# Performance work log

Hardware: AMD Instinct MI355X
Metric: run time of the kernel (lower is better)

Reference implementation:

```python
import jax, jax.numpy as jnp
import numpy as np

SCALING = 2.0  # alpha / r = 128 / 64


def setup_inputs() -> dict:
    key = jax.random.key(0)
    k1, k2, k3, k4 = jax.random.split(key, 4)
    in_f, out_f, r, tokens = 4096, 16384, 64, 64
    return {
        "x": jax.random.normal(k1, (tokens, in_f), dtype=jnp.float32),
        "weight": jax.random.normal(k2, (out_f, in_f), dtype=jnp.float32) * (1.0 / np.sqrt(in_f)),
        "lora_A": jax.random.normal(k3, (r, in_f), dtype=jnp.float32) * (1.0 / np.sqrt(in_f)),
        "lora_B": jax.random.normal(k4, (out_f, r), dtype=jnp.float32) * (1.0 / np.sqrt(r)),
    }


def reference(x, weight, lora_A, lora_B):
    # base GEMM: [T, in] @ [in, out] -> [T, out]
    base = x @ weight.T
    # low-rank adapter: ((x @ A^T) @ B^T) scaled
    lora = (x @ lora_A.T) @ lora_B.T
    return base + SCALING * lora
```

## Files before the change

kernel.cpp:

```cpp
#include <hip/hip_runtime.h>
#include <hip/hip_bf16.h>

typedef __attribute__((ext_vector_type(8))) short bf16x8;
typedef __attribute__((ext_vector_type(4))) float f32x4;

__device__ __forceinline__ short f2b(float f) {
    __hip_bfloat16 h = __float2bfloat16(f);
    return __builtin_bit_cast(short, h);
}

#define NPH 32
#define KC  128

__global__ void prep_kernel(const float* __restrict__ x,
                            const float* __restrict__ A,
                            ushort* __restrict__ xb,
                            ushort* __restrict__ yb) {
    const int tid = threadIdx.x, bid = blockIdx.x;

    const int gid = bid * 256 + tid;
    if (gid < 65536) {
        float4 v = ((const float4*)x)[gid];
        ushort4 s;
        s.x = (ushort)f2b(v.x); s.y = (ushort)f2b(v.y);
        s.z = (ushort)f2b(v.z); s.w = (ushort)f2b(v.w);
        ((ushort4*)xb)[gid] = s;
    }

    const int wave = tid >> 6, lane = tid & 63;
    const int idx = bid * 4 + wave;
    const int t = idx >> 6, r = idx & 63;
    const float4* xr = (const float4*)(x + (size_t)t * 4096);
    const float4* ar = (const float4*)(A + (size_t)r * 4096);
    float s = 0.f;
    #pragma unroll
    for (int i = 0; i < 16; ++i) {
        float4 a = xr[i * 64 + lane];
        float4 b = ar[i * 64 + lane];
        s += a.x * b.x + a.y * b.y + a.z * b.z + a.w * b.w;
    }
    #pragma unroll
    for (int off = 32; off; off >>= 1) s += __shfl_xor(s, off, 64);
    if (lane == 0) yb[idx] = (ushort)f2b(2.0f * s);
}

__global__ void __launch_bounds__(512)
lora_gemm(const float* __restrict__ W,
          const float* __restrict__ Bm,
          const ushort* __restrict__ xb,
          const ushort* __restrict__ yb,
          float* __restrict__ out) {
    __shared__ char buf[4][64 * 512];

    const int tid  = threadIdx.x;
    const int w    = tid >> 6;
    const int lane = tid & 63;
    const int j0   = blockIdx.x << 6;
    const int p0   = blockIdx.x & 31;

    if (w >= 4) {
        const int s = w - 4;
        auto issue = [&](int i) {
            const int p = (p0 + i) & 31;
            char* dst = &buf[i & 3][0];
            #pragma unroll
            for (int k = 0; k < 8; ++k) {
                const int qa = s * 16 + k * 2;
                const int q  = qa + (lane >> 5);
                const int b  = (lane & 31) * 16;
                const char* src = (const char*)(W + (size_t)(j0 + q) * 4096
                                                + (size_t)p * KC)
                                  + (b ^ ((q & 7) << 4));
                __builtin_amdgcn_global_load_lds(
                    (const uint32_t*)src,
                    (uint32_t*)(dst + qa * 512), 16, 0, 0);
            }
        };

        issue(0);
        issue(1);
        issue(2);
        for (int i = 0; i < NPH - 2; ++i) {
            asm volatile("s_waitcnt vmcnt(16)" ::: "memory");
            __builtin_amdgcn_s_barrier();
            if (i + 3 < NPH) issue(i + 3);
        }
        asm volatile("s_waitcnt vmcnt(8)" ::: "memory");
        __builtin_amdgcn_s_barrier();
        asm volatile("s_waitcnt vmcnt(0)" ::: "memory");
        __builtin_amdgcn_s_barrier();
        return;
    }

    const int c  = lane & 15;
    const int kg = lane >> 4;
    const ushort* xrow = xb + (size_t)(w * 16 + c) * 4096 + kg * 8;

    f32x4 acc[4];
    #pragma unroll
    for (int n = 0; n < 4; ++n) acc[n] = f32x4{0.f, 0.f, 0.f, 0.f};

    for (int i = 0; i < NPH; ++i) {
        const int p = (p0 + i) & 31;
        __builtin_amdgcn_s_barrier();
        const char* lb = &buf[i & 3][0];
        #pragma unroll
        for (int sl = 0; sl < 4; ++sl) {
            bf16x8 aa = *(const bf16x8*)(xrow + p * KC + sl * 32);
            #pragma unroll
            for (int n = 0; n < 4; ++n) {
                const int q   = n * 16 + c;
                const int swz = (q & 7) << 4;
                const char* base = lb + q * 512;
                f32x4 w0 = *(const f32x4*)(base + ((sl * 128 + kg * 32) ^ swz));
                f32x4 w1 = *(const f32x4*)(base + ((sl * 128 + kg * 32 + 16) ^ swz));
                bf16x8 bb;
                bb[0] = f2b(w0[0]); bb[1] = f2b(w0[1]);
                bb[2] = f2b(w0[2]); bb[3] = f2b(w0[3]);
                bb[4] = f2b(w1[0]); bb[5] = f2b(w1[1]);
                bb[6] = f2b(w1[2]); bb[7] = f2b(w1[3]);
                acc[n] = __builtin_amdgcn_mfma_f32_16x16x32_bf16(
                    aa, bb, acc[n], 0, 0, 0);
            }
        }
    }

    {
        const ushort* y0 = yb + (size_t)(w * 16 + c) * 64 + kg * 8;
        #pragma unroll
        for (int n = 0; n < 4; ++n) {
            const float* br = Bm + (size_t)(j0 + n * 16 + c) * 64 + kg * 8;
            #pragma unroll
            for (int k = 0; k < 64; k += 32) {
                f32x4 w0 = *(const f32x4*)(br + k);
                f32x4 w1 = *(const f32x4*)(br + k + 4);
                bf16x8 bb;
                bb[0] = f2b(w0[0]); bb[1] = f2b(w0[1]);
                bb[2] = f2b(w0[2]); bb[3] = f2b(w0[3]);
                bb[4] = f2b(w1[0]); bb[5] = f2b(w1[1]);
                bb[6] = f2b(w1[2]); bb[7] = f2b(w1[3]);
                bf16x8 aa = *(const bf16x8*)(y0 + k);
                acc[n] = __builtin_amdgcn_mfma_f32_16x16x32_bf16(
                    aa, bb, acc[n], 0, 0, 0);
            }
        }
    }

    #pragma unroll
    for (int n = 0; n < 4; ++n) {
        float* op = out + j0 + n * 16 + c;
        #pragma unroll
        for (int r = 0; r < 4; ++r)
            op[(size_t)(w * 16 + kg * 4 + r) * 16384] = acc[n][r];
    }
}

extern "C" void kernel_launch(void* const* d_in, const int* in_sizes, int n_in,
                              void* d_out, int out_size, void* d_ws, size_t ws_size,
                              hipStream_t stream) {
    const float* x  = (const float*)d_in[0];
    const float* W  = (const float*)d_in[1];
    const float* A  = (const float*)d_in[2];
    const float* Bm = (const float*)d_in[3];
    float* out = (float*)d_out;

    ushort* xb = (ushort*)d_ws;
    ushort* yb = (ushort*)((char*)d_ws + 524288);

    prep_kernel<<<1024, 256, 0, stream>>>(x, A, xb, yb);
    lora_gemm<<<256, 512, 0, stream>>>(W, Bm, xb, yb, out);
}
```

Measured before the change: 58.73 us.

## Stage W in 32-row by 1KB chunks instead of 64-row by 512B

Each pipeline stage now loads half of the 64 output rows (32 rows) over a 256-float K window, instead of all 64 rows over 128 floats. Each wave's global_load_lds now covers one contiguous 1KB row segment rather than two half-rows, which gives longer contiguous bursts per row and fewer DRAM page switches. Compute alternates between the two row halves, writing to acc[h*2+m], and the start-K rotation now spans 16 windows instead of 32. The accumulator index depends on the loop parity, which could cause dynamic register indexing unless the compiler unrolls the loop.

```diff
diff --git a/kernel.cpp b/kernel.cpp
--- a/kernel.cpp
+++ b/kernel.cpp
@@ -10,7 +10,7 @@
 }
 
 #define NPH 32
-#define KC  128
+#define KW  256
 
 __global__ void prep_kernel(const float* __restrict__ x,
                             const float* __restrict__ A,
@@ -50,30 +50,30 @@
           const ushort* __restrict__ xb,
           const ushort* __restrict__ yb,
           float* __restrict__ out) {
-    __shared__ char buf[4][64 * 512];
+    __shared__ char buf[4][32 * 1024];
 
     const int tid  = threadIdx.x;
     const int w    = tid >> 6;
     const int lane = tid & 63;
     const int j0   = blockIdx.x << 6;
-    const int p0   = blockIdx.x & 31;
+    const int p0   = blockIdx.x & 15;
 
     if (w >= 4) {
         const int s = w - 4;
         auto issue = [&](int i) {
-            const int p = (p0 + i) & 31;
+            const int kw = ((i >> 1) + p0) & 15;
+            const int h  = i & 1;
             char* dst = &buf[i & 3][0];
             #pragma unroll
             for (int k = 0; k < 8; ++k) {
-                const int qa = s * 16 + k * 2;
-                const int q  = qa + (lane >> 5);
-                const int b  = (lane & 31) * 16;
+                const int ri = s * 8 + k;
+                const int q  = h * 32 + ri;
                 const char* src = (const char*)(W + (size_t)(j0 + q) * 4096
-                                                + (size_t)p * KC)
-                                  + (b ^ ((q & 7) << 4));
+                                                + (size_t)kw * KW)
+                                  + ((lane * 16) ^ ((ri & 7) << 4));
                 __builtin_amdgcn_global_load_lds(
                     (const uint32_t*)src,
-                    (uint32_t*)(dst + qa * 512), 16, 0, 0);
+                    (uint32_t*)(dst + ri * 1024), 16, 0, 0);
             }
         };
 
@@ -101,17 +101,18 @@
     for (int n = 0; n < 4; ++n) acc[n] = f32x4{0.f, 0.f, 0.f, 0.f};
 
     for (int i = 0; i < NPH; ++i) {
-        const int p = (p0 + i) & 31;
+        const int kw = ((i >> 1) + p0) & 15;
+        const int h  = i & 1;
         __builtin_amdgcn_s_barrier();
         const char* lb = &buf[i & 3][0];
         #pragma unroll
-        for (int sl = 0; sl < 4; ++sl) {
-            bf16x8 aa = *(const bf16x8*)(xrow + p * KC + sl * 32);
+        for (int sl = 0; sl < 8; ++sl) {
+            bf16x8 aa = *(const bf16x8*)(xrow + kw * KW + sl * 32);
             #pragma unroll
-            for (int n = 0; n < 4; ++n) {
-                const int q   = n * 16 + c;
-                const int swz = (q & 7) << 4;
-                const char* base = lb + q * 512;
+            for (int m = 0; m < 2; ++m) {
+                const int ri  = m * 16 + c;
+                const int swz = (ri & 7) << 4;
+                const char* base = lb + ri * 1024;
                 f32x4 w0 = *(const f32x4*)(base + ((sl * 128 + kg * 32) ^ swz));
                 f32x4 w1 = *(const f32x4*)(base + ((sl * 128 + kg * 32 + 16) ^ swz));
                 bf16x8 bb;
@@ -119,8 +120,8 @@
                 bb[2] = f2b(w0[2]); bb[3] = f2b(w0[3]);
                 bb[4] = f2b(w1[0]); bb[5] = f2b(w1[1]);
                 bb[6] = f2b(w1[2]); bb[7] = f2b(w1[3]);
-                acc[n] = __builtin_amdgcn_mfma_f32_16x16x32_bf16(
-                    aa, bb, acc[n], 0, 0, 0);
+                acc[h * 2 + m] = __builtin_amdgcn_mfma_f32_16x16x32_bf16(
+                    aa, bb, acc[h * 2 + m], 0, 0, 0);
             }
         }
     }
```

Result: slower. 94.47 us (+60.9%).
